# Performance work log

Measured on AMD Instinct MI355X. Metric: run time of the kernel, lower is better.

## Reference

```python
import jax, jax.numpy as jnp
import numpy as np
from jax import lax

GAMMA_MIN = 1e-4
BIG = 1e9  # finite stand-in for +inf so softmin grads stay nan-free


def _cosine_cost(a, b):
    # F.normalize(dim=-1) with eps=1e-12, then 1 - a_n @ b_n.T
    an = a / jnp.maximum(jnp.linalg.norm(a, axis=-1, keepdims=True), 1e-12)
    bn = b / jnp.maximum(jnp.linalg.norm(b, axis=-1, keepdims=True), 1e-12)
    return 1.0 - an @ bn.T  # (M, N)


def _shift1(v):
    # v[i-1] with BIG padding at i=0
    return jnp.concatenate([jnp.full((1,), BIG, v.dtype), v[:-1]])


def _softdtw(cost, g):
    # Anti-diagonal wavefront DP. Diagonal d holds R[i, d-i], stored as a
    # length-(M+1) vector indexed by i. R[0,0]=0, borders = BIG (inf).
    M, N = cost.shape
    i_arr = jnp.arange(M + 1)
    r0 = jnp.full(M + 1, BIG, cost.dtype).at[0].set(0.0)  # diagonal d=0
    r1 = jnp.full(M + 1, BIG, cost.dtype)                 # diagonal d=1

    def step(carry, d):
        r_dm2, r_dm1 = carry  # diagonals d-2 and d-1
        j = d - i_arr
        valid = (i_arr >= 1) & (i_arr <= M) & (j >= 1) & (j <= N)
        c = cost[jnp.clip(i_arr - 1, 0, M - 1), jnp.clip(j - 1, 0, N - 1)]
        diag = _shift1(r_dm2)   # R[i-1, j-1]
        above = _shift1(r_dm1)  # R[i-1, j]
        left = r_dm1            # R[i,   j-1]
        v = jnp.stack([diag, above, left])  # (3, M+1)
        smin = -g * jax.nn.logsumexp(-v / g, axis=0)
        r_new = jnp.where(valid, c + smin, BIG)
        return (r_dm1, r_new), None

    ds = jnp.arange(2, M + N + 1)
    (_, r_last), _ = lax.scan(step, (r0, r1), ds)
    return r_last[M]  # R[M, N]


def setup_inputs() -> dict:
    key = jax.random.key(0)
    kx, ky = jax.random.split(key)
    M, N, D = 2048, 2048, 1024
    x = jax.random.normal(kx, (M, D), dtype=jnp.float32)
    y = jax.random.normal(ky, (N, D), dtype=jnp.float32)
    gamma = jnp.array(1.0, dtype=jnp.float32)  # learned nn.Parameter
    return {"x": x, "y": y, "gamma": gamma}


def reference(x, y, gamma):
    g = jnp.maximum(jnp.abs(gamma), GAMMA_MIN)
    sdtw = _softdtw(_cosine_cost(x, y), g)
    # normalize=True: subtract 0.5*(sdtw(x,x) + sdtw(y,y))
    sdtw_xx = _softdtw(_cosine_cost(x, x), g)
    sdtw_yy = _softdtw(_cosine_cost(y, y), g)
    return sdtw - 0.5 * (sdtw_xx + sdtw_yy)
```

## Files before the change

kernel.cpp:

```cpp
#include <hip/hip_runtime.h>
#include <hip/hip_bf16.h>
#include <math.h>

#define MDIM 2048
#define KDIM 1024
#define BIGF 1e9f
#define NSTRIP 16
#define DELTA 208
#define NPH 83

typedef unsigned short ushort;
typedef unsigned int uint;
typedef __attribute__((ext_vector_type(8))) short short8v;
typedef __attribute__((ext_vector_type(8))) ushort ushort8v;
typedef __attribute__((ext_vector_type(4))) float f32x4;

__device__ __forceinline__ ushort f2bf(float f) {
  uint b = __builtin_bit_cast(uint, f);
  b += 0x7FFFu + ((b >> 16) & 1u);
  return (ushort)(b >> 16);
}

__global__ __launch_bounds__(256) void normalize_rows(
    const float* __restrict__ x, const float* __restrict__ y,
    ushort* __restrict__ xb, ushort* __restrict__ yb) {
  int wave = (blockIdx.x * blockDim.x + threadIdx.x) >> 6;
  int lane = threadIdx.x & 63;
  const float* src;
  ushort* dst;
  int row;
  if (wave < MDIM) { src = x; dst = xb; row = wave; }
  else             { src = y; dst = yb; row = wave - MDIM; }
  const float* r = src + (size_t)row * KDIM;
  ushort* w = dst + (size_t)row * KDIM;
  float ss = 0.f;
  for (int c = lane * 4; c < KDIM; c += 64 * 4) {
    float4 v = *(const float4*)&r[c];
    ss += v.x * v.x + v.y * v.y + v.z * v.z + v.w * v.w;
  }
  #pragma unroll
  for (int off = 32; off; off >>= 1) ss += __shfl_xor(ss, off, 64);
  float inv = 1.f / fmaxf(sqrtf(ss), 1e-12f);
  for (int c = lane * 4; c < KDIM; c += 64 * 4) {
    float4 v = *(const float4*)&r[c];
    uint2 o;
    o.x = (uint)f2bf(v.x * inv) | ((uint)f2bf(v.y * inv) << 16);
    o.y = (uint)f2bf(v.z * inv) | ((uint)f2bf(v.w * inv) << 16);
    *(uint2*)&w[c] = o;
  }
}

__global__ __launch_bounds__(256) void gemm_cost_mfma(
    const ushort* __restrict__ xb, const ushort* __restrict__ yb,
    float* __restrict__ cost_base, const float* __restrict__ gamma_p) {
  int z = blockIdx.z;
  const ushort* A = (z == 2) ? yb : xb;
  const ushort* B = (z == 0) ? yb : ((z == 1) ? xb : yb);
  float* C = cost_base + (size_t)z * MDIM * MDIM;
  float g = fmaxf(fabsf(gamma_p[0]), 1e-4f);
  float kexp = 1.44269504089f / g;

  __shared__ ushort As[128 * 64];
  __shared__ ushort Bs[128 * 64];

  int tid = threadIdx.x;
  int w = tid >> 6, l = tid & 63;
  int wr = w >> 1, wc = w & 1;
  int abase = blockIdx.y * 128;
  int bbase = blockIdx.x * 128;

  f32x4 acc[4][4] = {};

  for (int k0 = 0; k0 < KDIM; k0 += 64) {
    ushort8v va[4], vb[4];
    #pragma unroll
    for (int q = 0; q < 4; ++q) {
      int slot = q * 256 + tid;
      int row = slot >> 3, sc = slot & 7;
      va[q] = *(const ushort8v*)&A[(size_t)(abase + row) * KDIM + k0 + sc * 8];
      vb[q] = *(const ushort8v*)&B[(size_t)(bbase + row) * KDIM + k0 + sc * 8];
    }
    __syncthreads();
    #pragma unroll
    for (int q = 0; q < 4; ++q) {
      int slot = q * 256 + tid;
      int row = slot >> 3, sc = slot & 7;
      int off = row * 64 + ((sc ^ (row & 7)) << 3);
      *(ushort8v*)&As[off] = va[q];
      *(ushort8v*)&Bs[off] = vb[q];
    }
    __syncthreads();
    #pragma unroll
    for (int kk = 0; kk < 2; ++kk) {
      short8v af[4], bf[4];
      #pragma unroll
      for (int m = 0; m < 4; ++m) {
        int row = wr * 64 + m * 16 + (l & 15);
        int kg = kk * 4 + (l >> 4);
        af[m] = *(const short8v*)&As[row * 64 + ((kg ^ (row & 7)) << 3)];
      }
      #pragma unroll
      for (int n = 0; n < 4; ++n) {
        int row = wc * 64 + n * 16 + (l & 15);
        int kg = kk * 4 + (l >> 4);
        bf[n] = *(const short8v*)&Bs[row * 64 + ((kg ^ (row & 7)) << 3)];
      }
      #pragma unroll
      for (int m = 0; m < 4; ++m)
        #pragma unroll
        for (int n = 0; n < 4; ++n)
          acc[m][n] = __builtin_amdgcn_mfma_f32_16x16x32_bf16(
              af[m], bf[n], acc[m][n], 0, 0, 0);
    }
  }
  #pragma unroll
  for (int m = 0; m < 4; ++m) {
    int row0 = abase + wr * 64 + m * 16 + (l >> 4) * 4;
    #pragma unroll
    for (int n = 0; n < 4; ++n) {
      int col = bbase + wc * 64 + n * 16 + (l & 15);
      f32x4 v = acc[m][n];
      #pragma unroll
      for (int r = 0; r < 4; ++r)
        C[(size_t)(row0 + r) * MDIM + col] = (1.0f - v[r]) * kexp;
    }
  }
}

__device__ __forceinline__ float fexp2(float x) { return __builtin_amdgcn_exp2f(x); }
__device__ __forceinline__ float flog2(float x) { return __builtin_amdgcn_logf(x); }

__device__ __forceinline__ float dpp_shr1(float v) {
  int r = __builtin_amdgcn_update_dpp(__builtin_bit_cast(int, v),
                                      __builtin_bit_cast(int, v),
                                      0x138 , 0xF, 0xF, false);
  return __builtin_bit_cast(float, r);
}

template <bool FIRST>
__device__ __forceinline__ void dp_phase_fast(
    float& o0, float& o1, float& d0, float& d1,
    float (&cq0)[16], float (&cq1)[16], float (&bq)[16],
    const float* c0p, const float* c1p, const float* bp, float* bw,
    int cb, int lane) {
  const bool l0 = (lane == 0);
  #pragma unroll 1
  for (int gq = 0; gq < 4; ++gq) {
    const int base = cb + gq * 16;
    const float* r0 = c0p + (base - 2 * lane + 16);
    const float* r1 = c1p + (base - 2 * lane + 15);
    const float* rb = bp + (base + 16);
    float* bwg = bw + (base - 127);
    float st[4];
    #pragma unroll
    for (int u = 0; u < 16; ++u) {
      float av0 = dpp_shr1(o1);
      av0 = l0 ? (FIRST ? BIGF : bq[u]) : av0;
      float av1 = o0;
      float mn0 = fminf(fminf(d0, av0), o0);
      float mn1 = fminf(fminf(d1, av1), o1);
      float e0 = fexp2(mn0 - d0) + fexp2(mn0 - av0) + fexp2(mn0 - o0);
      float e1 = fexp2(mn1 - d1) + fexp2(mn1 - av1) + fexp2(mn1 - o1);
      float n0 = cq0[u] + (mn0 - flog2(e0));
      float n1 = cq1[u] + (mn1 - flog2(e1));
      d0 = av0; d1 = av1; o0 = n0; o1 = n1;
      st[u & 3] = n1;
      if ((u & 3) == 3 && lane == 63) {
        float* a = bwg + (u - 3);
        a[0] = st[0]; a[1] = st[1]; a[2] = st[2]; a[3] = st[3];
      }
      cq0[u] = r0[u];
      cq1[u] = r1[u];
      bq[u] = FIRST ? BIGF : rb[u];
    }
  }
}

template <bool FIRST>
__device__ __forceinline__ void dp_phase_edge(
    float& o0, float& o1, float& d0, float& d1,
    float (&cq0)[16], float (&cq1)[16], float (&bq)[16],
    const float* c0p, const float* c1p, const float* bp, float* bw,
    int cb, int lane) {
  const bool l0 = (lane == 0);
  #pragma unroll 1
  for (int gq = 0; gq < 4; ++gq) {
    #pragma unroll
    for (int u = 0; u < 16; ++u) {
      int c0 = cb + gq * 16 + u - 2 * lane;
      int c1 = c0 - 1;
      float av0 = dpp_shr1(o1);
      if (FIRST) av0 = l0 ? ((c0 == -1) ? 0.0f : BIGF) : av0;
      else       av0 = l0 ? ((c0 < 0) ? BIGF : bq[u]) : av0;
      float av1 = o0;
      float mn0 = fminf(fminf(d0, av0), o0);
      float mn1 = fminf(fminf(d1, av1), o1);
      float e0 = fexp2(mn0 - d0) + fexp2(mn0 - av0) + fexp2(mn0 - o0);
      float e1 = fexp2(mn1 - d1) + fexp2(mn1 - av1) + fexp2(mn1 - o1);
      float n0 = cq0[u] + (mn0 - flog2(e0));
      float n1 = cq1[u] + (mn1 - flog2(e1));
      bool v0 = ((unsigned)c0 < (unsigned)MDIM);
      bool v1 = ((unsigned)c1 < (unsigned)MDIM);
      n0 = v0 ? n0 : BIGF;
      n1 = v1 ? n1 : BIGF;
      d0 = av0; d1 = av1; o0 = n0; o1 = n1;
      if (v1 && lane == 63) bw[c1] = n1;
      int q0 = min(max(c0 + 16, 0), MDIM - 1);
      int q1 = min(max(c1 + 16, 0), MDIM - 1);
      int qb = min(max(cb + gq * 16 + u + 16, 0), MDIM - 1);
      cq0[u] = c0p[q0];
      cq1[u] = c1p[q1];
      bq[u] = FIRST ? BIGF : bp[qb];
    }
  }
}

__global__ __launch_bounds__(64) void softdtw_dp(
    const float* __restrict__ cost_base, float* __restrict__ bottom,
    int* __restrict__ flags) {
  const int s = blockIdx.x;
  const int z = blockIdx.y;
  const int lane = threadIdx.x;
  const float* cost = cost_base + (size_t)z * MDIM * MDIM;
  float* bot_z = bottom + (size_t)z * NSTRIP * MDIM;

  const float* c0p = cost + (size_t)(s * 128 + 2 * lane) * MDIM;
  const float* c1p = c0p + MDIM;
  const float* bp = bot_z + (size_t)((s > 0 ? s : 1) - 1) * MDIM;
  float* bw = bot_z + (size_t)s * MDIM;

  const int pS0 = (DELTA * s) >> 6;
  const int pS1 = (DELTA * s + 2174) >> 6;

  int* predf = &flags[z * NSTRIP + (s > 0 ? s - 1 : 0)];
  int* myf = &flags[z * NSTRIP + s];

  float o0 = BIGF, o1 = BIGF, d0 = BIGF, d1 = BIGF;
  float cq0[16], cq1[16], bq[16];

  for (int p = 0; p < NPH; ++p) {
    if (s > 0) {
      int it = 0;
      while (__hip_atomic_load(predf, __ATOMIC_ACQUIRE,
                               __HIP_MEMORY_SCOPE_AGENT) < p) {
        __builtin_amdgcn_s_sleep(1);
        if (++it > (1 << 22)) break;
      }
    }
    if (p >= pS0 && p <= pS1) {
      const int cb = 64 * p - DELTA * s;
      if (p == pS0) {
        o0 = o1 = d1 = BIGF;
        d0 = (s == 0 && lane == 0) ? 0.0f : BIGF;
        #pragma unroll
        for (int u = 0; u < 16; ++u) {
          int q0 = min(max(cb + u - 2 * lane, 0), MDIM - 1);
          int q1 = min(max(cb + u - 2 * lane - 1, 0), MDIM - 1);
          int qb = min(max(cb + u, 0), MDIM - 1);
          cq0[u] = c0p[q0];
          cq1[u] = c1p[q1];
          bq[u] = (s == 0) ? BIGF : bp[qb];
        }
      }
      bool interior = (64 * p >= DELTA * s + 127) && (64 * p <= DELTA * s + 1968);
      if (s == 0) {
        if (interior)
          dp_phase_fast<true>(o0, o1, d0, d1, cq0, cq1, bq, c0p, c1p, bp, bw, cb, lane);
        else
          dp_phase_edge<true>(o0, o1, d0, d1, cq0, cq1, bq, c0p, c1p, bp, bw, cb, lane);
      } else {
        if (interior)
          dp_phase_fast<false>(o0, o1, d0, d1, cq0, cq1, bq, c0p, c1p, bp, bw, cb, lane);
        else
          dp_phase_edge<false>(o0, o1, d0, d1, cq0, cq1, bq, c0p, c1p, bp, bw, cb, lane);
      }
    }
    if (lane == 63)
      __hip_atomic_store(myf, p + 1, __ATOMIC_RELEASE,
                         __HIP_MEMORY_SCOPE_AGENT);
  }
}

__global__ void dtw_init(int* __restrict__ flags) {
  if (threadIdx.x < 3 * NSTRIP) flags[threadIdx.x] = 0;
}

__global__ void combine(const float* __restrict__ bottom,
                        const float* __restrict__ gamma_p,
                        float* __restrict__ out) {
  float g = fmaxf(fabsf(gamma_p[0]), 1e-4f);
  float glog = 0.69314718056f * g;
  float b0 = bottom[0 * NSTRIP * MDIM + 15 * MDIM + 2047];
  float b1 = bottom[1 * NSTRIP * MDIM + 15 * MDIM + 2047];
  float b2 = bottom[2 * NSTRIP * MDIM + 15 * MDIM + 2047];
  out[0] = (b0 - 0.5f * (b1 + b2)) * glog;
}

extern "C" void kernel_launch(void* const* d_in, const int* in_sizes, int n_in,
                              void* d_out, int out_size, void* d_ws, size_t ws_size,
                              hipStream_t stream) {
  const float* x = (const float*)d_in[0];
  const float* y = (const float*)d_in[1];
  const float* gamma = (const float*)d_in[2];
  float* out = (float*)d_out;

  char* ws = (char*)d_ws;
  ushort* xb = (ushort*)ws;
  ushort* yb = (ushort*)(ws + (size_t)4 * 1024 * 1024);
  float* cost = (float*)(ws + (size_t)8 * 1024 * 1024);
  float* bottom = (float*)(ws + (size_t)56 * 1024 * 1024);
  int* flags = (int*)(ws + (size_t)57 * 1024 * 1024);

  normalize_rows<<<(2 * MDIM) / 4, 256, 0, stream>>>(x, y, xb, yb);

  dim3 ggrid(MDIM / 128, MDIM / 128, 3);
  gemm_cost_mfma<<<ggrid, 256, 0, stream>>>(xb, yb, cost, gamma);

  dtw_init<<<1, 64, 0, stream>>>(flags);

  dim3 dgrid(NSTRIP, 3);
  softdtw_dp<<<dgrid, 64, 0, stream>>>(cost, bottom, flags);

  combine<<<1, 1, 0, stream>>>(bottom, gamma, out);
}
```

Before: 793.3 us.

## Stage cost tiles in LDS with ring buffer and finer-grained wavefront phases

Reworks the soft-DTW wavefront kernel so each strip stages its cost tile into a 64KB LDS ring buffer ahead of use, replacing per-step scattered global loads. Phases are halved to 32 columns to shorten the pipeline fill between strips, and the row mapping changes from two adjacent rows per lane to rows lane and lane+64 using a rotate DPP. The logsumexp now uses min/med3/max so one exp becomes the constant 1, and blocks are spread across a 128-block grid with one block per CU. The costs are more synchronisation phases and more complex indexing, with correctness depending on the slot arithmetic.

```diff
diff --git a/kernel.cpp b/kernel.cpp
--- a/kernel.cpp
+++ b/kernel.cpp
@@ -6,14 +6,15 @@
 #define KDIM 1024
 #define BIGF 1e9f
 #define NSTRIP 16
-#define DELTA 208
-#define NPH 83
+#define DELTA 192
+#define NPH 158
 
 typedef unsigned short ushort;
 typedef unsigned int uint;
 typedef __attribute__((ext_vector_type(8))) short short8v;
 typedef __attribute__((ext_vector_type(8))) ushort ushort8v;
 typedef __attribute__((ext_vector_type(4))) float f32x4;
+typedef __attribute__((ext_vector_type(4))) float fvec4;
 
 __device__ __forceinline__ ushort f2bf(float f) {
   uint b = __builtin_bit_cast(uint, f);
@@ -130,149 +131,203 @@
 __device__ __forceinline__ float fexp2(float x) { return __builtin_amdgcn_exp2f(x); }
 __device__ __forceinline__ float flog2(float x) { return __builtin_amdgcn_logf(x); }
 
-__device__ __forceinline__ float dpp_shr1(float v) {
+__device__ __forceinline__ float ror1(float v) {
   int r = __builtin_amdgcn_update_dpp(__builtin_bit_cast(int, v),
                                       __builtin_bit_cast(int, v),
-                                      0x138 , 0xF, 0xF, false);
+                                      0x13C , 0xF, 0xF, false);
   return __builtin_bit_cast(float, r);
 }
 
-template <bool FIRST>
-__device__ __forceinline__ void dp_phase_fast(
-    float& o0, float& o1, float& d0, float& d1,
-    float (&cq0)[16], float (&cq1)[16], float (&bq)[16],
-    const float* c0p, const float* c1p, const float* bp, float* bw,
-    int cb, int lane) {
+__device__ __forceinline__ float aload(const float* p) {
+  return __hip_atomic_load(p, __ATOMIC_RELAXED, __HIP_MEMORY_SCOPE_AGENT);
+}
+
+template <bool FIRST, bool EDGE>
+__device__ __forceinline__ void dp_group16(
+    float& o0, float& o1, float& d0, float& d1, float& cc0, float& cc1,
+    float (&bq)[16], const float* __restrict__ bp, float* __restrict__ bw,
+    const float* smem, int cb16, int lane, int ln32) {
   const bool l0 = (lane == 0);
-  #pragma unroll 1
-  for (int gq = 0; gq < 4; ++gq) {
-    const int base = cb + gq * 16;
-    const float* r0 = c0p + (base - 2 * lane + 16);
-    const float* r1 = c1p + (base - 2 * lane + 15);
-    const float* rb = bp + (base + 16);
-    float* bwg = bw + (base - 127);
-    float st[4];
-    #pragma unroll
-    for (int u = 0; u < 16; ++u) {
-      float av0 = dpp_shr1(o1);
-      av0 = l0 ? (FIRST ? BIGF : bq[u]) : av0;
-      float av1 = o0;
-      float mn0 = fminf(fminf(d0, av0), o0);
-      float mn1 = fminf(fminf(d1, av1), o1);
-      float e0 = fexp2(mn0 - d0) + fexp2(mn0 - av0) + fexp2(mn0 - o0);
-      float e1 = fexp2(mn1 - d1) + fexp2(mn1 - av1) + fexp2(mn1 - o1);
-      float n0 = cq0[u] + (mn0 - flog2(e0));
-      float n1 = cq1[u] + (mn1 - flog2(e1));
-      d0 = av0; d1 = av1; o0 = n0; o1 = n1;
-      st[u & 3] = n1;
-      if ((u & 3) == 3 && lane == 63) {
-        float* a = bwg + (u - 3);
-        a[0] = st[0]; a[1] = st[1]; a[2] = st[2]; a[3] = st[3];
-      }
-      cq0[u] = r0[u];
-      cq1[u] = r1[u];
-      bq[u] = FIRST ? BIGF : rb[u];
-    }
-  }
-}
-
-template <bool FIRST>
-__device__ __forceinline__ void dp_phase_edge(
-    float& o0, float& o1, float& d0, float& d1,
-    float (&cq0)[16], float (&cq1)[16], float (&bq)[16],
-    const float* c0p, const float* c1p, const float* bp, float* bw,
-    int cb, int lane) {
-  const bool l0 = (lane == 0);
-  #pragma unroll 1
-  for (int gq = 0; gq < 4; ++gq) {
-    #pragma unroll
-    for (int u = 0; u < 16; ++u) {
-      int c0 = cb + gq * 16 + u - 2 * lane;
-      int c1 = c0 - 1;
-      float av0 = dpp_shr1(o1);
-      if (FIRST) av0 = l0 ? ((c0 == -1) ? 0.0f : BIGF) : av0;
-      else       av0 = l0 ? ((c0 < 0) ? BIGF : bq[u]) : av0;
-      float av1 = o0;
-      float mn0 = fminf(fminf(d0, av0), o0);
-      float mn1 = fminf(fminf(d1, av1), o1);
-      float e0 = fexp2(mn0 - d0) + fexp2(mn0 - av0) + fexp2(mn0 - o0);
-      float e1 = fexp2(mn1 - d1) + fexp2(mn1 - av1) + fexp2(mn1 - o1);
-      float n0 = cq0[u] + (mn0 - flog2(e0));
-      float n1 = cq1[u] + (mn1 - flog2(e1));
-      bool v0 = ((unsigned)c0 < (unsigned)MDIM);
+  const bool l63 = (lane == 63);
+  const int K = cb16 - lane;
+  float h0, h1, h2, h3;
+  #pragma unroll
+  for (int u = 0; u < 16; ++u) {
+    int nrel = K + u + 1;
+    int xx = nrel & 31;
+    int sl = (nrel >> 5) & 3;
+    float p0 = smem[(sl << 11) + ln32 + xx];
+    float p1 = smem[8192 + (((sl ^ 2) & 3) << 11) + ln32 + xx];
+    float t0 = ror1(o0);
+    float t1 = ror1(o1);
+    float av0 = FIRST ? (l0 ? BIGF : t0) : (l0 ? bq[u] : t0);
+    float av1 = l0 ? t0 : t1;
+    float mn0 = fminf(fminf(d0, av0), o0);
+    float mx0 = fmaxf(fmaxf(d0, av0), o0);
+    float md0;
+    asm("v_med3_f32 %0, %1, %2, %3" : "=v"(md0) : "v"(d0), "v"(av0), "v"(o0));
+    float mn1 = fminf(fminf(d1, av1), o1);
+    float mx1 = fmaxf(fmaxf(d1, av1), o1);
+    float md1;
+    asm("v_med3_f32 %0, %1, %2, %3" : "=v"(md1) : "v"(d1), "v"(av1), "v"(o1));
+    float e0 = 1.0f + fexp2(mn0 - md0) + fexp2(mn0 - mx0);
+    float e1 = 1.0f + fexp2(mn1 - md1) + fexp2(mn1 - mx1);
+    float n0 = cc0 + (mn0 - flog2(e0));
+    float n1 = cc1 + (mn1 - flog2(e1));
+    if (EDGE) {
+      int c0 = K + u;
+      int c1 = c0 - 64;
+      n0 = ((unsigned)c0 < (unsigned)MDIM) ? n0 : BIGF;
       bool v1 = ((unsigned)c1 < (unsigned)MDIM);
-      n0 = v0 ? n0 : BIGF;
       n1 = v1 ? n1 : BIGF;
-      d0 = av0; d1 = av1; o0 = n0; o1 = n1;
-      if (v1 && lane == 63) bw[c1] = n1;
-      int q0 = min(max(c0 + 16, 0), MDIM - 1);
-      int q1 = min(max(c1 + 16, 0), MDIM - 1);
-      int qb = min(max(cb + gq * 16 + u + 16, 0), MDIM - 1);
-      cq0[u] = c0p[q0];
-      cq1[u] = c1p[q1];
-      bq[u] = FIRST ? BIGF : bp[qb];
-    }
-  }
-}
-
-__global__ __launch_bounds__(64) void softdtw_dp(
+      if (l63 && v1) bw[c1] = n1;
+    } else {
+      if ((u & 3) == 0) h0 = n1;
+      else if ((u & 3) == 1) h1 = n1;
+      else if ((u & 3) == 2) h2 = n1;
+      else h3 = n1;
+      if ((u & 3) == 3 && l63) {
+        float* a = &bw[cb16 + u - 130];
+        a[0] = h0; a[1] = h1; a[2] = h2; a[3] = h3;
+      }
+    }
+    d0 = av0; d1 = av1; o0 = n0; o1 = n1;
+    cc0 = p0; cc1 = p1;
+    if (!FIRST) {
+      int qb = cb16 + u + 16;
+      if (EDGE) qb = min(max(qb, 0), MDIM - 1);
+      bq[u] = aload(&bp[qb]);
+    }
+  }
+}
+
+template <bool FIRST, bool EDGE>
+__device__ __forceinline__ void dp_phase(
+    float& o0, float& o1, float& d0, float& d1, float& cc0, float& cc1,
+    float (&bq)[16], const float* __restrict__ bp, float* __restrict__ bw,
+    float* smem, const float* __restrict__ cost_s,
+    int cb, int lane, int ln32, bool do_stage, int slotA, int slotB) {
+  fvec4 sA[8], sB[8];
+  const int f4c = lane & 7;
+  const int rsub = lane >> 3;
+  if (do_stage) {
+    int cA = min(max(cb + 32 + f4c * 4, 0), MDIM - 4);
+    int cB = min(max(cb - 32 + f4c * 4, 0), MDIM - 4);
+    #pragma unroll
+    for (int k = 0; k < 8; ++k) {
+      sA[k] = *(const fvec4*)&cost_s[(size_t)(k * 8 + rsub) * MDIM + cA];
+      sB[k] = *(const fvec4*)&cost_s[(size_t)(64 + k * 8 + rsub) * MDIM + cB];
+    }
+  }
+  dp_group16<FIRST, EDGE>(o0, o1, d0, d1, cc0, cc1, bq, bp, bw, smem,
+                          cb, lane, ln32);
+  if (do_stage) {
+    #pragma unroll
+    for (int k = 0; k < 8; ++k) {
+      int ro = (k * 8 + rsub) * 32 + f4c * 4;
+      *(fvec4*)&smem[slotA * 2048 + ro] = sA[k];
+      *(fvec4*)&smem[8192 + slotB * 2048 + ro] = sB[k];
+    }
+  }
+  dp_group16<FIRST, EDGE>(o0, o1, d0, d1, cc0, cc1, bq, bp, bw, smem,
+                          cb + 16, lane, ln32);
+}
+
+__global__ __launch_bounds__(64, 1) void softdtw_dp(
     const float* __restrict__ cost_base, float* __restrict__ bottom,
     int* __restrict__ flags) {
-  const int s = blockIdx.x;
-  const int z = blockIdx.y;
+  extern __shared__ float smem[];
+  const int bid = blockIdx.x;
+  const int z = bid & 7;
+  if (z >= 3) return;
+  const int s = bid >> 3;
   const int lane = threadIdx.x;
+  const int ln32 = lane * 32;
+
   const float* cost = cost_base + (size_t)z * MDIM * MDIM;
+  const float* cost_s = cost + (size_t)s * 128 * MDIM;
   float* bot_z = bottom + (size_t)z * NSTRIP * MDIM;
-
-  const float* c0p = cost + (size_t)(s * 128 + 2 * lane) * MDIM;
-  const float* c1p = c0p + MDIM;
-  const float* bp = bot_z + (size_t)((s > 0 ? s : 1) - 1) * MDIM;
+  const float* bp = bot_z + (size_t)(s > 0 ? s - 1 : 0) * MDIM;
   float* bw = bot_z + (size_t)s * MDIM;
-
-  const int pS0 = (DELTA * s) >> 6;
-  const int pS1 = (DELTA * s + 2174) >> 6;
-
   int* predf = &flags[z * NSTRIP + (s > 0 ? s - 1 : 0)];
   int* myf = &flags[z * NSTRIP + s];
 
-  float o0 = BIGF, o1 = BIGF, d0 = BIGF, d1 = BIGF;
-  float cq0[16], cq1[16], bq[16];
+  const int pS0 = 6 * s;
+  const int pS1 = (DELTA * s + 2174) >> 5;
+
+  {
+    const int f4c = lane & 7;
+    const int rsub = lane >> 3;
+    #pragma unroll
+    for (int q = 0; q < 3; ++q) {
+      int colA = (q - 2) * 32;
+      int colB = (q - 4) * 32;
+      int cA = min(max(colA + f4c * 4, 0), MDIM - 4);
+      int cB = min(max(colB + f4c * 4, 0), MDIM - 4);
+      int slA = (q - 2) & 3;
+      int slB = (q - 4) & 3;
+      fvec4 vA[8], vB[8];
+      #pragma unroll
+      for (int k = 0; k < 8; ++k) {
+        vA[k] = *(const fvec4*)&cost_s[(size_t)(k * 8 + rsub) * MDIM + cA];
+        vB[k] = *(const fvec4*)&cost_s[(size_t)(64 + k * 8 + rsub) * MDIM + cB];
+      }
+      #pragma unroll
+      for (int k = 0; k < 8; ++k) {
+        int ro = (k * 8 + rsub) * 32 + f4c * 4;
+        *(fvec4*)&smem[slA * 2048 + ro] = vA[k];
+        *(fvec4*)&smem[8192 + slB * 2048 + ro] = vB[k];
+      }
+    }
+  }
+
+  float o0 = BIGF, o1 = BIGF, d0 = BIGF, d1 = BIGF, cc0 = 0.f, cc1 = 0.f;
+  float bq[16];
+  int pcache = 0;
 
   for (int p = 0; p < NPH; ++p) {
-    if (s > 0) {
+    if (s > 0 && pcache < p) {
       int it = 0;
-      while (__hip_atomic_load(predf, __ATOMIC_ACQUIRE,
-                               __HIP_MEMORY_SCOPE_AGENT) < p) {
-        __builtin_amdgcn_s_sleep(1);
-        if (++it > (1 << 22)) break;
-      }
+      do {
+        pcache = __hip_atomic_load(predf, __ATOMIC_ACQUIRE,
+                                   __HIP_MEMORY_SCOPE_AGENT);
+        if (pcache < p) __builtin_amdgcn_s_sleep(1);
+      } while (pcache < p && ++it < (1 << 22));
     }
     if (p >= pS0 && p <= pS1) {
-      const int cb = 64 * p - DELTA * s;
+      const int dq = p - pS0;
+      const int cb = dq << 5;
       if (p == pS0) {
         o0 = o1 = d1 = BIGF;
         d0 = (s == 0 && lane == 0) ? 0.0f : BIGF;
-        #pragma unroll
-        for (int u = 0; u < 16; ++u) {
-          int q0 = min(max(cb + u - 2 * lane, 0), MDIM - 1);
-          int q1 = min(max(cb + u - 2 * lane - 1, 0), MDIM - 1);
-          int qb = min(max(cb + u, 0), MDIM - 1);
-          cq0[u] = c0p[q0];
-          cq1[u] = c1p[q1];
-          bq[u] = (s == 0) ? BIGF : bp[qb];
+        int nrel = -lane;
+        int xx = nrel & 31;
+        int sl = (nrel >> 5) & 3;
+        cc0 = smem[(sl << 11) + ln32 + xx];
+        cc1 = smem[8192 + (((sl ^ 2) & 3) << 11) + ln32 + xx];
+        if (s > 0) {
+          #pragma unroll
+          for (int u = 0; u < 16; ++u) bq[u] = aload(&bp[u]);
         }
       }
-      bool interior = (64 * p >= DELTA * s + 127) && (64 * p <= DELTA * s + 1968);
+      const bool do_stage = p < pS1;
+      const bool interior = (cb >= 128) && (cb <= 2016);
+      const int slotA = (dq + 1) & 3;
+      const int slotB = (dq - 1) & 3;
       if (s == 0) {
         if (interior)
-          dp_phase_fast<true>(o0, o1, d0, d1, cq0, cq1, bq, c0p, c1p, bp, bw, cb, lane);
+          dp_phase<true, false>(o0, o1, d0, d1, cc0, cc1, bq, bp, bw, smem,
+                                cost_s, cb, lane, ln32, do_stage, slotA, slotB);
         else
-          dp_phase_edge<true>(o0, o1, d0, d1, cq0, cq1, bq, c0p, c1p, bp, bw, cb, lane);
+          dp_phase<true, true>(o0, o1, d0, d1, cc0, cc1, bq, bp, bw, smem,
+                               cost_s, cb, lane, ln32, do_stage, slotA, slotB);
       } else {
         if (interior)
-          dp_phase_fast<false>(o0, o1, d0, d1, cq0, cq1, bq, c0p, c1p, bp, bw, cb, lane);
+          dp_phase<false, false>(o0, o1, d0, d1, cc0, cc1, bq, bp, bw, smem,
+                                 cost_s, cb, lane, ln32, do_stage, slotA, slotB);
         else
-          dp_phase_edge<false>(o0, o1, d0, d1, cq0, cq1, bq, c0p, c1p, bp, bw, cb, lane);
+          dp_phase<false, true>(o0, o1, d0, d1, cc0, cc1, bq, bp, bw, smem,
+                                cost_s, cb, lane, ln32, do_stage, slotA, slotB);
       }
     }
     if (lane == 63)
@@ -318,8 +373,7 @@
 
   dtw_init<<<1, 64, 0, stream>>>(flags);
 
-  dim3 dgrid(NSTRIP, 3);
-  softdtw_dp<<<dgrid, 64, 0, stream>>>(cost, bottom, flags);
+  softdtw_dp<<<128, 64, 65536, stream>>>(cost, bottom, flags);
 
   combine<<<1, 1, 0, stream>>>(bottom, gamma, out);
 }
```

New measurement: 995.8 us. +25.5%, slower.

## Restructure soft-DTW wavefront to one row per lane with 32 strips

Applied to the files above, without the earlier changes.

The DP kernel now assigns one row per lane (64 rows per strip, 32 strips) instead of two rows per lane across 16 strips. This shortens the serial chain per step and pipelines strips with a two-phase lag. Cost rows are double-buffered in registers with vector loads. The predecessor strip's boundary row comes in through one load plus readlane broadcasts. The soft-min uses min3/med3/max3 so one exponential drops out. The grid is spread over 256 blocks so each strip lands on its own CU. In exchange there are more inter-block flag handshakes and high register pressure from the two 64-float buffers.

```diff
diff --git a/kernel.cpp b/kernel.cpp
--- a/kernel.cpp
+++ b/kernel.cpp
@@ -5,15 +5,14 @@
 #define MDIM 2048
 #define KDIM 1024
 #define BIGF 1e9f
-#define NSTRIP 16
-#define DELTA 208
-#define NPH 83
+#define NSTRIP 32
 
 typedef unsigned short ushort;
 typedef unsigned int uint;
 typedef __attribute__((ext_vector_type(8))) short short8v;
 typedef __attribute__((ext_vector_type(8))) ushort ushort8v;
 typedef __attribute__((ext_vector_type(4))) float f32x4;
+typedef __attribute__((ext_vector_type(4), aligned(4))) float f4u;
 
 __device__ __forceinline__ ushort f2bf(float f) {
   uint b = __builtin_bit_cast(uint, f);
@@ -130,155 +129,151 @@
 __device__ __forceinline__ float fexp2(float x) { return __builtin_amdgcn_exp2f(x); }
 __device__ __forceinline__ float flog2(float x) { return __builtin_amdgcn_logf(x); }
 
-__device__ __forceinline__ float dpp_shr1(float v) {
+__device__ __forceinline__ float shr1(float v) {
   int r = __builtin_amdgcn_update_dpp(__builtin_bit_cast(int, v),
                                       __builtin_bit_cast(int, v),
                                       0x138 , 0xF, 0xF, false);
   return __builtin_bit_cast(float, r);
 }
 
-template <bool FIRST>
-__device__ __forceinline__ void dp_phase_fast(
-    float& o0, float& o1, float& d0, float& d1,
-    float (&cq0)[16], float (&cq1)[16], float (&bq)[16],
-    const float* c0p, const float* c1p, const float* bp, float* bw,
-    int cb, int lane) {
+__device__ __forceinline__ float aload(const float* p) {
+  return __hip_atomic_load(p, __ATOMIC_RELAXED, __HIP_MEMORY_SCOPE_AGENT);
+}
+
+__device__ __forceinline__ void stage(f4u (&buf)[16],
+                                      const float* __restrict__ crow, int base) {
+  #pragma unroll
+  for (int k = 0; k < 16; ++k)
+    buf[k] = *(const f4u*)&crow[base + 4 * k];
+}
+
+__device__ __forceinline__ void stage_edge(f4u (&buf)[16],
+                                           const float* __restrict__ crow,
+                                           int base) {
+  #pragma unroll
+  for (int k = 0; k < 16; ++k)
+    #pragma unroll
+    for (int j = 0; j < 4; ++j) {
+      int col = min(max(base + 4 * k + j, 0), MDIM - 1);
+      buf[k][j] = crow[col];
+    }
+}
+
+template <bool FIRST, bool EDGE>
+__device__ __forceinline__ void phase_body(
+    float& o, float& d, float bqv, const f4u (&cur)[16],
+    int cb, int lane, float* __restrict__ bw) {
   const bool l0 = (lane == 0);
-  #pragma unroll 1
-  for (int gq = 0; gq < 4; ++gq) {
-    const int base = cb + gq * 16;
-    const float* r0 = c0p + (base - 2 * lane + 16);
-    const float* r1 = c1p + (base - 2 * lane + 15);
-    const float* rb = bp + (base + 16);
-    float* bwg = bw + (base - 127);
-    float st[4];
-    #pragma unroll
-    for (int u = 0; u < 16; ++u) {
-      float av0 = dpp_shr1(o1);
-      av0 = l0 ? (FIRST ? BIGF : bq[u]) : av0;
-      float av1 = o0;
-      float mn0 = fminf(fminf(d0, av0), o0);
-      float mn1 = fminf(fminf(d1, av1), o1);
-      float e0 = fexp2(mn0 - d0) + fexp2(mn0 - av0) + fexp2(mn0 - o0);
-      float e1 = fexp2(mn1 - d1) + fexp2(mn1 - av1) + fexp2(mn1 - o1);
-      float n0 = cq0[u] + (mn0 - flog2(e0));
-      float n1 = cq1[u] + (mn1 - flog2(e1));
-      d0 = av0; d1 = av1; o0 = n0; o1 = n1;
-      st[u & 3] = n1;
-      if ((u & 3) == 3 && lane == 63) {
-        float* a = bwg + (u - 3);
-        a[0] = st[0]; a[1] = st[1]; a[2] = st[2]; a[3] = st[3];
-      }
-      cq0[u] = r0[u];
-      cq1[u] = r1[u];
-      bq[u] = FIRST ? BIGF : rb[u];
-    }
-  }
-}
-
-template <bool FIRST>
-__device__ __forceinline__ void dp_phase_edge(
-    float& o0, float& o1, float& d0, float& d1,
-    float (&cq0)[16], float (&cq1)[16], float (&bq)[16],
-    const float* c0p, const float* c1p, const float* bp, float* bw,
-    int cb, int lane) {
-  const bool l0 = (lane == 0);
-  #pragma unroll 1
-  for (int gq = 0; gq < 4; ++gq) {
-    #pragma unroll
-    for (int u = 0; u < 16; ++u) {
-      int c0 = cb + gq * 16 + u - 2 * lane;
-      int c1 = c0 - 1;
-      float av0 = dpp_shr1(o1);
-      if (FIRST) av0 = l0 ? ((c0 == -1) ? 0.0f : BIGF) : av0;
-      else       av0 = l0 ? ((c0 < 0) ? BIGF : bq[u]) : av0;
-      float av1 = o0;
-      float mn0 = fminf(fminf(d0, av0), o0);
-      float mn1 = fminf(fminf(d1, av1), o1);
-      float e0 = fexp2(mn0 - d0) + fexp2(mn0 - av0) + fexp2(mn0 - o0);
-      float e1 = fexp2(mn1 - d1) + fexp2(mn1 - av1) + fexp2(mn1 - o1);
-      float n0 = cq0[u] + (mn0 - flog2(e0));
-      float n1 = cq1[u] + (mn1 - flog2(e1));
-      bool v0 = ((unsigned)c0 < (unsigned)MDIM);
-      bool v1 = ((unsigned)c1 < (unsigned)MDIM);
-      n0 = v0 ? n0 : BIGF;
-      n1 = v1 ? n1 : BIGF;
-      d0 = av0; d1 = av1; o0 = n0; o1 = n1;
-      if (v1 && lane == 63) bw[c1] = n1;
-      int q0 = min(max(c0 + 16, 0), MDIM - 1);
-      int q1 = min(max(c1 + 16, 0), MDIM - 1);
-      int qb = min(max(cb + gq * 16 + u + 16, 0), MDIM - 1);
-      cq0[u] = c0p[q0];
-      cq1[u] = c1p[q1];
-      bq[u] = FIRST ? BIGF : bp[qb];
-    }
-  }
-}
-
-__global__ __launch_bounds__(64) void softdtw_dp(
+  const bool l63 = (lane == 63);
+  float h0, h1, h2, h3;
+  #pragma unroll
+  for (int u = 0; u < 64; ++u) {
+    float t = shr1(o);
+    float av;
+    if (FIRST) {
+      av = l0 ? BIGF : t;
+    } else {
+      float rv = __builtin_bit_cast(
+          float, __builtin_amdgcn_readlane(__builtin_bit_cast(int, bqv), u));
+      av = l0 ? rv : t;
+    }
+    float mn, md, mx;
+    asm("v_min3_f32 %0, %1, %2, %3" : "=v"(mn) : "v"(d), "v"(av), "v"(o));
+    asm("v_med3_f32 %0, %1, %2, %3" : "=v"(md) : "v"(d), "v"(av), "v"(o));
+    asm("v_max3_f32 %0, %1, %2, %3" : "=v"(mx) : "v"(d), "v"(av), "v"(o));
+    float e = 1.0f + fexp2(mn - md) + fexp2(mn - mx);
+    float n = cur[u >> 2][u & 3] + (mn - flog2(e));
+    if (EDGE) {
+      int c = cb + u - lane;
+      bool valid = ((unsigned)c < (unsigned)MDIM);
+      n = valid ? n : BIGF;
+      if (l63 && valid) bw[c] = n;
+    } else {
+      if ((u & 3) == 0) h0 = n;
+      else if ((u & 3) == 1) h1 = n;
+      else if ((u & 3) == 2) h2 = n;
+      else {
+        h3 = n;
+        if (l63) *(f4u*)&bw[cb + u - 66] = (f4u){h0, h1, h2, h3};
+      }
+    }
+    d = av;
+    o = n;
+  }
+}
+
+__global__ __launch_bounds__(64, 1) void softdtw_dp(
     const float* __restrict__ cost_base, float* __restrict__ bottom,
     int* __restrict__ flags) {
-  const int s = blockIdx.x;
-  const int z = blockIdx.y;
+  const int bid = blockIdx.x;
+  const int z = bid & 7;
+  if (z >= 3) return;
+  const int s = bid >> 3;
   const int lane = threadIdx.x;
+
   const float* cost = cost_base + (size_t)z * MDIM * MDIM;
+  const float* crow = cost + (size_t)(s * 64 + lane) * MDIM;
   float* bot_z = bottom + (size_t)z * NSTRIP * MDIM;
-
-  const float* c0p = cost + (size_t)(s * 128 + 2 * lane) * MDIM;
-  const float* c1p = c0p + MDIM;
-  const float* bp = bot_z + (size_t)((s > 0 ? s : 1) - 1) * MDIM;
+  const float* bp = bot_z + (size_t)(s > 0 ? s - 1 : 0) * MDIM;
   float* bw = bot_z + (size_t)s * MDIM;
-
-  const int pS0 = (DELTA * s) >> 6;
-  const int pS1 = (DELTA * s + 2174) >> 6;
-
   int* predf = &flags[z * NSTRIP + (s > 0 ? s - 1 : 0)];
   int* myf = &flags[z * NSTRIP + s];
 
-  float o0 = BIGF, o1 = BIGF, d0 = BIGF, d1 = BIGF;
-  float cq0[16], cq1[16], bq[16];
-
-  for (int p = 0; p < NPH; ++p) {
-    if (s > 0) {
+  const int pS0 = 2 * s;
+  const int pS1 = 2 * s + 32;
+
+  f4u bufA[16], bufB[16];
+  stage_edge(bufA, crow, -lane);
+
+  float o = BIGF;
+  float d = (s == 0 && lane == 0) ? 0.0f : BIGF;
+
+  if (lane == 63 && s > 0)
+    __hip_atomic_store(myf, pS0, __ATOMIC_RELEASE, __HIP_MEMORY_SCOPE_AGENT);
+
+  int pcache = 0;
+  for (int p = pS0; p <= pS1; ++p) {
+    const int dq = p - pS0;
+    const int cb = dq << 6;
+    if (s > 0 && pcache < p) {
       int it = 0;
-      while (__hip_atomic_load(predf, __ATOMIC_ACQUIRE,
-                               __HIP_MEMORY_SCOPE_AGENT) < p) {
-        __builtin_amdgcn_s_sleep(1);
-        if (++it > (1 << 22)) break;
-      }
-    }
-    if (p >= pS0 && p <= pS1) {
-      const int cb = 64 * p - DELTA * s;
-      if (p == pS0) {
-        o0 = o1 = d1 = BIGF;
-        d0 = (s == 0 && lane == 0) ? 0.0f : BIGF;
-        #pragma unroll
-        for (int u = 0; u < 16; ++u) {
-          int q0 = min(max(cb + u - 2 * lane, 0), MDIM - 1);
-          int q1 = min(max(cb + u - 2 * lane - 1, 0), MDIM - 1);
-          int qb = min(max(cb + u, 0), MDIM - 1);
-          cq0[u] = c0p[q0];
-          cq1[u] = c1p[q1];
-          bq[u] = (s == 0) ? BIGF : bp[qb];
-        }
-      }
-      bool interior = (64 * p >= DELTA * s + 127) && (64 * p <= DELTA * s + 1968);
-      if (s == 0) {
-        if (interior)
-          dp_phase_fast<true>(o0, o1, d0, d1, cq0, cq1, bq, c0p, c1p, bp, bw, cb, lane);
-        else
-          dp_phase_edge<true>(o0, o1, d0, d1, cq0, cq1, bq, c0p, c1p, bp, bw, cb, lane);
+      do {
+        pcache = __hip_atomic_load(predf, __ATOMIC_ACQUIRE,
+                                   __HIP_MEMORY_SCOPE_AGENT);
+        if (pcache < p) __builtin_amdgcn_s_sleep(1);
+      } while (pcache < p && ++it < (1 << 22));
+    }
+    float bqv = 0.0f;
+    if (s > 0) bqv = aload(&bp[min(cb + lane, MDIM - 1)]);
+    if (dq < 31) {
+      if ((dq & 1) == 0) stage(bufB, crow, cb + 64 - lane);
+      else               stage(bufA, crow, cb + 64 - lane);
+    } else if (dq == 31) {
+      stage_edge(bufA, crow, cb + 64 - lane);
+    }
+    const bool edge = (dq == 0) || (dq == 32);
+    if (s == 0) {
+      if ((dq & 1) == 0) {
+        if (edge) phase_body<true, true>(o, d, bqv, bufA, cb, lane, bw);
+        else      phase_body<true, false>(o, d, bqv, bufA, cb, lane, bw);
       } else {
-        if (interior)
-          dp_phase_fast<false>(o0, o1, d0, d1, cq0, cq1, bq, c0p, c1p, bp, bw, cb, lane);
-        else
-          dp_phase_edge<false>(o0, o1, d0, d1, cq0, cq1, bq, c0p, c1p, bp, bw, cb, lane);
+        phase_body<true, false>(o, d, bqv, bufB, cb, lane, bw);
+      }
+    } else {
+      if ((dq & 1) == 0) {
+        if (edge) phase_body<false, true>(o, d, bqv, bufA, cb, lane, bw);
+        else      phase_body<false, false>(o, d, bqv, bufA, cb, lane, bw);
+      } else {
+        phase_body<false, false>(o, d, bqv, bufB, cb, lane, bw);
       }
     }
     if (lane == 63)
       __hip_atomic_store(myf, p + 1, __ATOMIC_RELEASE,
                          __HIP_MEMORY_SCOPE_AGENT);
   }
+  if (lane == 63)
+    __hip_atomic_store(myf, 1 << 20, __ATOMIC_RELEASE,
+                       __HIP_MEMORY_SCOPE_AGENT);
 }
 
 __global__ void dtw_init(int* __restrict__ flags) {
@@ -290,9 +285,9 @@
                         float* __restrict__ out) {
   float g = fmaxf(fabsf(gamma_p[0]), 1e-4f);
   float glog = 0.69314718056f * g;
-  float b0 = bottom[0 * NSTRIP * MDIM + 15 * MDIM + 2047];
-  float b1 = bottom[1 * NSTRIP * MDIM + 15 * MDIM + 2047];
-  float b2 = bottom[2 * NSTRIP * MDIM + 15 * MDIM + 2047];
+  float b0 = bottom[0 * NSTRIP * MDIM + (NSTRIP - 1) * MDIM + 2047];
+  float b1 = bottom[1 * NSTRIP * MDIM + (NSTRIP - 1) * MDIM + 2047];
+  float b2 = bottom[2 * NSTRIP * MDIM + (NSTRIP - 1) * MDIM + 2047];
   out[0] = (b0 - 0.5f * (b1 + b2)) * glog;
 }
 
@@ -309,17 +304,16 @@
   ushort* yb = (ushort*)(ws + (size_t)4 * 1024 * 1024);
   float* cost = (float*)(ws + (size_t)8 * 1024 * 1024);
   float* bottom = (float*)(ws + (size_t)56 * 1024 * 1024);
-  int* flags = (int*)(ws + (size_t)57 * 1024 * 1024);
+  int* flags = (int*)(ws + (size_t)59 * 1024 * 1024);
 
   normalize_rows<<<(2 * MDIM) / 4, 256, 0, stream>>>(x, y, xb, yb);
 
   dim3 ggrid(MDIM / 128, MDIM / 128, 3);
   gemm_cost_mfma<<<ggrid, 256, 0, stream>>>(xb, yb, cost, gamma);
 
-  dtw_init<<<1, 64, 0, stream>>>(flags);
-
-  dim3 dgrid(NSTRIP, 3);
-  softdtw_dp<<<dgrid, 64, 0, stream>>>(cost, bottom, flags);
+  dtw_init<<<1, 128, 0, stream>>>(flags);
+
+  softdtw_dp<<<256, 64, 0, stream>>>(cost, bottom, flags);
 
   combine<<<1, 1, 0, stream>>>(bottom, gamma, out);
 }
```

Result: slower. 887.0 us (+11.8%).
